# Kernel optimization log

Measured on AMD Instinct MI355X. Metric: run time of the kernel, lower is better.

Reference implementation:

```python
import jax, jax.numpy as jnp
import numpy as np

NUM_DISPARITIES = 48
IS_RIGHT = False
CLAMP = 1000.0


def setup_inputs() -> dict:
    key = jax.random.key(0)
    k1, k2 = jax.random.split(key)
    B, C, H, W = 2, 32, 136, 240
    left = jax.random.normal(k1, (B, C, H, W), dtype=jnp.float32)
    right = jax.random.normal(k2, (B, C, H, W), dtype=jnp.float32)
    return {"left": left, "right": right}


def reference(left, right):
    # Faithful to cost_volume(left, right, NUM_DISPARITIES, IS_RIGHT) followed by
    # the float32 cast + clamp(-1000, 1000) from forward_with_amp.
    left = left.astype(jnp.float32)
    right = right.astype(jnp.float32)
    B, C, H, W = left.shape
    D = NUM_DISPARITIES
    d = jnp.arange(D)[:, None]        # (D, 1)
    w = jnp.arange(W)[None, :]        # (1, W)
    if not IS_RIGHT:
        # out[b,c,i,h,w] = left[b,c,h,w] * right[b,c,h,w-i] for w >= i else 0
        src = w - d                   # (D, W) index into right along width
        valid = src >= 0
        gathered = jnp.take(right, jnp.clip(src, 0, W - 1), axis=3)  # (B,C,H,D,W)
        gathered = jnp.moveaxis(gathered, 3, 2)                      # (B,C,D,H,W)
        out = left[:, :, None, :, :] * gathered
    else:
        # out[b,c,i,h,w] = left[b,c,h,w+i] * right[b,c,h,w] for w < W-i else 0
        src = w + d                   # (D, W) index into left along width
        valid = src <= W - 1
        gathered = jnp.take(left, jnp.clip(src, 0, W - 1), axis=3)   # (B,C,H,D,W)
        gathered = jnp.moveaxis(gathered, 3, 2)                      # (B,C,D,H,W)
        out = gathered * right[:, :, None, :, :]
    out = jnp.where(valid[None, None, :, None, :], out, jnp.float32(0.0))
    return jnp.clip(out, -CLAMP, CLAMP)
```

## Files before the change

### kernel.cpp

```cpp
#include <hip/hip_runtime.h>
#include <hip/hip_bf16.h>

constexpr int B = 2, C = 32, H = 136, W = 240, D = 48;
constexpr int W4      = W / 4;
constexpr int PLANE   = H * W;
constexpr int PLANE4  = PLANE / 4;
constexpr int NPLANES = B * C * D;
constexpr float CLAMP = 1000.0f;

typedef float v4f __attribute__((ext_vector_type(4)));

__device__ __forceinline__ float clampv(float x) {
    return fminf(CLAMP, fmaxf(-CLAMP, x));
}

__global__ __launch_bounds__(256) void CostVolume_4939212390829_kernel(
        const float* __restrict__ left,
        const float* __restrict__ right,
        float* __restrict__ out) {
    const int p  = blockIdx.x;
    const int bc = p / D;
    const int d  = p % D;

    const float* __restrict__ lplane = left  + (size_t)bc * PLANE;
    const float* __restrict__ rplane = right + (size_t)bc * PLANE;
    float* __restrict__ oplane = out + (size_t)p * PLANE;

    for (int i = threadIdx.x; i < PLANE4; i += 256) {
        const int h = i / W4;
        const int w = (i - h * W4) * 4;
        const int row = h * W;

        const v4f l4 = *(const v4f*)(lplane + row + w);

        const float* __restrict__ rrow = rplane + row + (w - d);
        float r0 = (w + 0 >= d) ? rrow[0] : 0.0f;
        float r1 = (w + 1 >= d) ? rrow[1] : 0.0f;
        float r2 = (w + 2 >= d) ? rrow[2] : 0.0f;
        float r3 = (w + 3 >= d) ? rrow[3] : 0.0f;

        v4f o4;
        o4.x = clampv(l4.x * r0);
        o4.y = clampv(l4.y * r1);
        o4.z = clampv(l4.z * r2);
        o4.w = clampv(l4.w * r3);

        __builtin_nontemporal_store(o4, (v4f*)(oplane + i * 4));
    }
}

extern "C" void kernel_launch(void* const* d_in, const int* in_sizes, int n_in,
                              void* d_out, int out_size, void* d_ws, size_t ws_size,
                              hipStream_t stream) {
    const float* left  = (const float*)d_in[0];
    const float* right = (const float*)d_in[1];
    float* out = (float*)d_out;
    (void)in_sizes; (void)n_in; (void)out_size; (void)d_ws; (void)ws_size;

    CostVolume_4939212390829_kernel<<<NPLANES, 256, 0, stream>>>(left, right, out);
}
```

Measured before the change: 496.4 us.

## Stage right rows in LDS and compute four disparities per block

Each block now handles four consecutive disparities for one (b,c) plane, loading quarter-plane tiles of the right image into zero-padded shared memory. Unaligned disparity shifts are built from two aligned vector LDS reads instead of four masked scalar global loads. This aims to cut redundant global reads and address arithmetic. In exchange it adds block-wide barriers and repeated shared-memory staging per phase, and it drops the nontemporal store hint.

```diff
diff --git a/kernel.cpp b/kernel.cpp
--- a/kernel.cpp
+++ b/kernel.cpp
@@ -1,52 +1,87 @@
 #include <hip/hip_runtime.h>
-#include <hip/hip_bf16.h>
 
 constexpr int B = 2, C = 32, H = 136, W = 240, D = 48;
-constexpr int W4      = W / 4;
 constexpr int PLANE   = H * W;
 constexpr int PLANE4  = PLANE / 4;
-constexpr int NPLANES = B * C * D;
-constexpr float CLAMP = 1000.0f;
+constexpr int QROWS   = 34;
+constexpr int NQ      = H / QROWS;
+constexpr int QSLOTS  = QROWS * W / 4;
+constexpr int DPB     = 4;
+constexpr int NBLK    = B * C * (D / DPB);
+constexpr int LROW16  = 73;
+constexpr float CLAMPV = 1000.0f;
 
 typedef float v4f __attribute__((ext_vector_type(4)));
 
 __device__ __forceinline__ float clampv(float x) {
-    return fminf(CLAMP, fmaxf(-CLAMP, x));
+    return fminf(CLAMPV, fmaxf(-CLAMPV, x));
+}
+__device__ __forceinline__ int div60(int s) { return (s * 2185) >> 17; }
+
+template<int J>
+__device__ __forceinline__ void phaseJ(v4f* __restrict__ sR,
+                                       const v4f* __restrict__ lp4,
+                                       const v4f* __restrict__ rp4,
+                                       v4f* __restrict__ op4,
+                                       int d4, int tid) {
+    for (int q = 0; q < NQ; ++q) {
+        __syncthreads();
+        for (int i = tid; i < QSLOTS; i += 512) {
+            const int r = div60(i);
+            sR[r * LROW16 + 13 + (i - 60 * r)] = rp4[q * QSLOTS + i];
+        }
+        __syncthreads();
+        #pragma unroll
+        for (int it = 0; it < 4; ++it) {
+            const int s = tid + 512 * it;
+            if (s < QSLOTS) {
+                const int r  = div60(s);
+                const int c4 = s - 60 * r;
+                const int t  = r * LROW16 + 13 + c4 - d4;
+                const v4f l4 = lp4[q * QSLOTS + s];
+                const v4f Q  = sR[t];
+                v4f w;
+                if constexpr (J == 0) {
+                    w = Q;
+                } else {
+                    const v4f X = sR[t - 1];
+                    if constexpr (J == 1)      { w.x=X.w; w.y=Q.x; w.z=Q.y; w.w=Q.z; }
+                    else if constexpr (J == 2) { w.x=X.z; w.y=X.w; w.z=Q.x; w.w=Q.y; }
+                    else                       { w.x=X.y; w.y=X.z; w.z=X.w; w.w=Q.x; }
+                }
+                v4f o;
+                o.x = clampv(l4.x * w.x); o.y = clampv(l4.y * w.y);
+                o.z = clampv(l4.z * w.z); o.w = clampv(l4.w * w.w);
+                op4[q * QSLOTS + s] = o;
+            }
+        }
+    }
 }
 
-__global__ __launch_bounds__(256) void CostVolume_4939212390829_kernel(
+__global__ __launch_bounds__(512) void CostVolume_4939212390829_kernel(
         const float* __restrict__ left,
         const float* __restrict__ right,
         float* __restrict__ out) {
-    const int p  = blockIdx.x;
-    const int bc = p / D;
-    const int d  = p % D;
+    const int blk = blockIdx.x;
+    const int bc  = blk / (D / DPB);
+    const int d4  = blk - bc * (D / DPB);
+    const int tid = threadIdx.x;
 
-    const float* __restrict__ lplane = left  + (size_t)bc * PLANE;
-    const float* __restrict__ rplane = right + (size_t)bc * PLANE;
-    float* __restrict__ oplane = out + (size_t)p * PLANE;
+    __shared__ v4f sR[QROWS * LROW16];
 
-    for (int i = threadIdx.x; i < PLANE4; i += 256) {
-        const int h = i / W4;
-        const int w = (i - h * W4) * 4;
-        const int row = h * W;
+    const v4f* __restrict__ lp4 = (const v4f*)left  + (size_t)bc * PLANE4;
+    const v4f* __restrict__ rp4 = (const v4f*)right + (size_t)bc * PLANE4;
+    v4f* __restrict__ op4 = (v4f*)out + ((size_t)bc * D + 4 * d4) * PLANE4;
 
-        const v4f l4 = *(const v4f*)(lplane + row + w);
+    if (tid < QROWS * 13) {
+        const int r = tid / 13, c = tid - 13 * r;
+        sR[r * LROW16 + c] = (v4f){0.f, 0.f, 0.f, 0.f};
+    }
 
-        const float* __restrict__ rrow = rplane + row + (w - d);
-        float r0 = (w + 0 >= d) ? rrow[0] : 0.0f;
-        float r1 = (w + 1 >= d) ? rrow[1] : 0.0f;
-        float r2 = (w + 2 >= d) ? rrow[2] : 0.0f;
-        float r3 = (w + 3 >= d) ? rrow[3] : 0.0f;
-
-        v4f o4;
-        o4.x = clampv(l4.x * r0);
-        o4.y = clampv(l4.y * r1);
-        o4.z = clampv(l4.z * r2);
-        o4.w = clampv(l4.w * r3);
-
-        __builtin_nontemporal_store(o4, (v4f*)(oplane + i * 4));
-    }
+    phaseJ<0>(sR, lp4, rp4, op4,              d4, tid);
+    phaseJ<1>(sR, lp4, rp4, op4 +     PLANE4, d4, tid);
+    phaseJ<2>(sR, lp4, rp4, op4 + 2 * PLANE4, d4, tid);
+    phaseJ<3>(sR, lp4, rp4, op4 + 3 * PLANE4, d4, tid);
 }
 
 extern "C" void kernel_launch(void* const* d_in, const int* in_sizes, int n_in,
@@ -57,5 +92,5 @@
     float* out = (float*)d_out;
     (void)in_sizes; (void)n_in; (void)out_size; (void)d_ws; (void)ws_size;
 
-    CostVolume_4939212390829_kernel<<<NPLANES, 256, 0, stream>>>(left, right, out);
+    CostVolume_4939212390829_kernel<<<NBLK, 512, 0, stream>>>(left, right, out);
 }
```

New measurement: 456.6 us. -8.0%, faster.
